# Kernel tuning notes

Hardware: AMD Instinct MI355X
Metric: run time of the kernel (lower is better)

The kernel has to match this reference:

```python
import jax, jax.numpy as jnp
import numpy as np

B, N, X, H = 128, 1023, 256, 256  # N = 2**(D+1)-1 perfect binary trees, root at 0


def _lin_init(key, out_d, in_d, scale=None):
    if scale is None:
        scale = 1.0 / np.sqrt(in_d)
    kw, kb = jax.random.split(key)
    W = jax.random.uniform(kw, (out_d, in_d), jnp.float32, -scale, scale)
    b = jax.random.uniform(kb, (out_d,), jnp.float32, -scale, scale)
    return W, b


def setup_inputs() -> dict:
    key = jax.random.key(0)
    ks = jax.random.split(key, 16)
    embed = jax.random.normal(ks[0], (B, N, X), jnp.float32)
    Wf, bf = _lin_init(ks[1], H, X + H)
    Wi, bi = _lin_init(ks[2], H, X + H)
    Wu, bu = _lin_init(ks[3], H, X + H)
    Wo, bo = _lin_init(ks[4], H, X + H)
    # extra nn.Parameter biases, initialized to zeros as in the module
    b_f = jnp.zeros((H,), jnp.float32)
    b_i = jnp.zeros((H,), jnp.float32)
    b_u = jnp.zeros((H,), jnp.float32)
    b_o = jnp.zeros((H,), jnp.float32)
    W1, bl1 = _lin_init(ks[5], H, H)
    W2, bl2 = _lin_init(ks[6], H, H)
    W3, bl3 = _lin_init(ks[7], H, H)
    W4, bl4 = _lin_init(ks[8], H, H)
    return {"embed": embed, "Wf": Wf, "bf": bf, "b_f": b_f, "Wi": Wi, "bi": bi,
            "b_i": b_i, "Wu": Wu, "bu": bu, "b_u": b_u, "Wo": Wo, "bo": bo,
            "b_o": b_o, "W1": W1, "bl1": bl1, "W2": W2, "bl2": bl2,
            "W3": W3, "bl3": bl3, "W4": W4, "bl4": bl4}


def _tree_lstm(embed, Wf, bf, b_f, Wi, bi, b_i, Wu, bu, b_u, Wo, bo, b_o):
    Bn, Nn, Xn = embed.shape
    Hn = Wf.shape[0]
    D = int(np.log2(Nn + 1)) - 1  # leaf level index
    h = jnp.zeros((Bn, Nn, Hn), embed.dtype)
    c = jnp.zeros((Bn, Nn, Hn), embed.dtype)
    # initial (leaf) level: no children -> h_sum = 0, c_tilde = 0 (apply_node_func on init state)
    i_g = jax.nn.sigmoid(bi + b_i)
    u_g = jnp.tanh(bu + b_u)
    c_leaf = i_g * u_g
    h_leaf = jax.nn.sigmoid(bo + b_o) * jnp.tanh(c_leaf)
    ls, lc = 2 ** D - 1, 2 ** D
    h = h.at[:, ls:ls + lc].set(jnp.broadcast_to(h_leaf, (Bn, lc, Hn)))
    c = c.at[:, ls:ls + lc].set(jnp.broadcast_to(c_leaf, (Bn, lc, Hn)))
    # level-by-level leaf->root; children of node n are 2n+1, 2n+2 (contiguous per level)
    for l in range(D - 1, -1, -1):
        s, cnt = 2 ** l - 1, 2 ** l
        cs, ccnt = 2 ** (l + 1) - 1, 2 ** (l + 1)
        ch_h = h[:, cs:cs + ccnt]        # [B, 2*cnt, H]
        ch_c = c[:, cs:cs + ccnt]
        ch_e = embed[:, cs:cs + ccnt]
        # message: cat([h, embed]); reduce: sum over the 2 children
        msg = jnp.concatenate([ch_h, ch_e], axis=-1).reshape(Bn, cnt, 2, Hn + Xn)
        h_sum = msg.sum(axis=2)                                   # [B, cnt, H+X]
        c_sum = ch_c.reshape(Bn, cnt, 2, Hn).sum(axis=2)          # [B, cnt, H]
        f = jax.nn.sigmoid(h_sum @ Wf.T + bf + b_f)
        c_tilde = f * c_sum  # f broadcast over children: f*(c1+c2) == sum_k f*c_k
        i_gate = jax.nn.sigmoid(h_sum @ Wi.T + bi + b_i)
        u = jnp.tanh(h_sum @ Wu.T + bu + b_u)
        c_new = i_gate * u + c_tilde
        o = jax.nn.sigmoid(h_sum @ Wo.T + bo + b_o)
        h_new = o * jnp.tanh(c_new)
        h = h.at[:, s:s + cnt].set(h_new)
        c = c.at[:, s:s + cnt].set(c_new)
    return h[:, 0]  # root hidden state, [B, H]


def reference(embed, Wf, bf, b_f, Wi, bi, b_i, Wu, bu, b_u, Wo, bo, b_o,
              W1, bl1, W2, bl2, W3, bl3, W4, bl4):
    hr = _tree_lstm(embed, Wf, bf, b_f, Wi, bi, b_i, Wu, bu, b_u, Wo, bo, b_o)
    # dropout is identity in eval mode
    y = jnp.tanh(hr @ W1.T + bl1)
    y2 = jax.nn.relu(hr @ W2.T + bl2) @ W3.T + bl3
    return jax.nn.relu((y + y2) @ W4.T + bl4)
```

## Files before the change

### kernel.cpp

```cpp
#include <hip/hip_runtime.h>

#define HD 256
#define KD 512

typedef _Float16 half8 __attribute__((ext_vector_type(8)));
typedef _Float16 half2v __attribute__((ext_vector_type(2)));
typedef _Float16 half4v __attribute__((ext_vector_type(4)));
typedef float floatx4 __attribute__((ext_vector_type(4)));
typedef float floatx2 __attribute__((ext_vector_type(2)));

__device__ __forceinline__ float sigmf_(float x) { return 1.f / (1.f + __expf(-x)); }
__device__ __forceinline__ float tanhf_(float x) {
  x = fminf(fmaxf(x, -15.f), 15.f);
  float e = __expf(2.f * x);
  return (e - 1.f) / (e + 1.f);
}

__global__ void prep_kernel(const float* __restrict__ bf_, const float* __restrict__ b_f,
                            const float* __restrict__ bi_, const float* __restrict__ b_i,
                            const float* __restrict__ bu_, const float* __restrict__ b_u,
                            const float* __restrict__ bo_, const float* __restrict__ b_o,
                            const float* __restrict__ Wf, const float* __restrict__ Wi,
                            const float* __restrict__ Wu, const float* __restrict__ Wo,
                            float* __restrict__ bsum, float* __restrict__ bias2,
                            float* __restrict__ cleaf2)
{
  __shared__ float hl2[HD];
  __shared__ float part[64][4];
  const int t = threadIdx.x;
  float sf = bf_[t] + b_f[t];
  float si = bi_[t] + b_i[t];
  float su = bu_[t] + b_u[t];
  float so = bo_[t] + b_o[t];
  float ig = 1.f / (1.f + expf(-si));
  float uu = tanhf(su);
  float cl = ig * uu;
  float hl = (1.f / (1.f + expf(-so))) * tanhf(cl);
  hl2[t] = 2.f * hl;
  if (blockIdx.x == 0) {
    bsum[t] = sf; bsum[HD + t] = si; bsum[2 * HD + t] = su; bsum[3 * HD + t] = so;
    cleaf2[t] = cl + cl;
  }
  __syncthreads();
  const int g = blockIdx.x >> 2, q = blockIdx.x & 3;
  const int nl = t >> 2, kq = t & 3;
  const float* Wg = (g == 0) ? Wf : (g == 1) ? Wi : (g == 2) ? Wu : Wo;
  const float* w = Wg + (long)(q * 64 + nl) * KD + kq * 64;
  float s = 0.f;
  for (int k = 0; k < 64; k += 4) {
    floatx4 wv = *(const floatx4*)(w + k);
    floatx4 hv = *(const floatx4*)(&hl2[kq * 64 + k]);
    s += wv[0] * hv[0] + wv[1] * hv[1] + wv[2] * hv[2] + wv[3] * hv[3];
  }
  part[nl][kq] = s;
  __syncthreads();
  if (kq == 0) {
    const int n = q * 64 + nl;
    float tot = part[nl][0] + part[nl][1] + part[nl][2] + part[nl][3];
    float bg = (g == 0) ? (bf_[n] + b_f[n]) : (g == 1) ? (bi_[n] + b_i[n])
             : (g == 2) ? (bu_[n] + b_u[n]) : (bo_[n] + b_o[n]);
    bias2[g * HD + n] = bg + tot;
  }
}

__global__ void wcvt_kernel(const float* __restrict__ Wf, const float* __restrict__ Wi,
                            const float* __restrict__ Wu, const float* __restrict__ Wo,
                            _Float16* __restrict__ Wh)
{
  int idx = (blockIdx.x * 256 + threadIdx.x) * 4;
  int g = idx >> 17;
  int rem = idx & ((1 << 17) - 1);
  const float* src = (g == 0) ? Wf : (g == 1) ? Wi : (g == 2) ? Wu : Wo;
  floatx4 v = *(const floatx4*)(src + rem);
  half4v o;
  o[0] = (_Float16)v[0]; o[1] = (_Float16)v[1]; o[2] = (_Float16)v[2]; o[3] = (_Float16)v[3];
  *(half4v*)(Wh + idx) = o;
}

__global__ void esum_kernel(const float* __restrict__ embed, _Float16* __restrict__ esum)
{
  const int task = blockIdx.x * 256 + threadIdx.x;
  if (task >= 511 * 32) return;
  const int b = blockIdx.y;
  const int p = task >> 5, g8 = task & 31;
  const float* e0 = embed + ((long)b * 1023 + 2 * p + 1) * 256 + g8 * 8;
  const float* e1 = e0 + 256;
  floatx4 x0 = *(const floatx4*)(e0);
  floatx4 x1 = *(const floatx4*)(e0 + 4);
  floatx4 y0 = *(const floatx4*)(e1);
  floatx4 y1 = *(const floatx4*)(e1 + 4);
  half8 s;
#pragma unroll
  for (int e = 0; e < 4; ++e) { s[e] = (_Float16)(x0[e] + y0[e]); s[4 + e] = (_Float16)(x1[e] + y1[e]); }
  *(half8*)(esum + ((long)b * 511 + p) * 256 + g8 * 8) = s;
}

__global__ __launch_bounds__(256, 2)
void level_kernel(const _Float16* __restrict__ hsum_in,
                  const float* __restrict__ csum_in,
                  const _Float16* __restrict__ esum,
                  const _Float16* __restrict__ Wh,
                  const float* __restrict__ bias,
                  _Float16* __restrict__ hsum_out,
                  float* __restrict__ csum_out,
                  int l, int leaf, int fin)
{
  __shared__ _Float16 As[128][256];

  const int cb = blockIdx.y;
  const int m0 = blockIdx.x * 128;
  const int t = threadIdx.x;
  const int wave = t >> 6;
  const int lane = t & 63;
  const int lm = lane & 15;
  const int quad = lane >> 4;
  const int rh = wave >> 1;
  const int ch = wave & 1;
  const int ncol = cb * 32 + ch * 16 + lm;

  floatx4 acc[4][4] = {};

  const int srow0 = t >> 3;
  const int sg = t & 7;

  const _Float16* wb = Wh + (long)ncol * KD + quad * 8;

  auto gemm_chunk = [&](int kbase) {
    half8 bcur[4], bnxt[4];
#pragma unroll
    for (int g = 0; g < 4; ++g)
      bcur[g] = *(const half8*)(wb + (long)g * HD * KD + kbase);
#pragma unroll
    for (int ks = 0; ks < 8; ++ks) {
      if (ks < 7) {
#pragma unroll
        for (int g = 0; g < 4; ++g)
          bnxt[g] = *(const half8*)(wb + (long)g * HD * KD + kbase + (ks + 1) * 32);
      }
      half8 afr[4];
#pragma unroll
      for (int mt = 0; mt < 4; ++mt) {
        int row = rh * 64 + mt * 16 + lm;
        afr[mt] = *(const half8*)(&As[row][(((ks * 4 + quad) ^ (row & 7)) * 8)]);
      }
#pragma unroll
      for (int mt = 0; mt < 4; ++mt)
#pragma unroll
        for (int g = 0; g < 4; ++g)
          acc[mt][g] = __builtin_amdgcn_mfma_f32_16x16x32_f16(afr[mt], bcur[g], acc[mt][g], 0, 0, 0);
#pragma unroll
      for (int g = 0; g < 4; ++g) bcur[g] = bnxt[g];
    }
  };

  const int msk = (1 << l) - 1;

  if (!leaf) {
#pragma unroll
    for (int p = 0; p < 4; ++p) {
      const int r = srow0 + 32 * p;
      const _Float16* src = hsum_in + (long)(m0 + r) * HD;
#pragma unroll
      for (int q = 0; q < 4; ++q) {
        int g8 = sg + 8 * q;
        *(half8*)(&As[r][((g8 ^ (r & 7)) * 8)]) = *(const half8*)(src + g8 * 8);
      }
    }
    __syncthreads();
    gemm_chunk(0);
    __syncthreads();
  }

  {
#pragma unroll
    for (int p = 0; p < 4; ++p) {
      const int r = srow0 + 32 * p;
      const int sm = m0 + r;
      const long erow = (long)(sm >> l) * 511 + msk + (sm & msk);
      const _Float16* src = esum + erow * HD;
#pragma unroll
      for (int q = 0; q < 4; ++q) {
        int g8 = sg + 8 * q;
        *(half8*)(&As[r][((g8 ^ (r & 7)) * 8)]) = *(const half8*)(src + g8 * 8);
      }
    }
  }
  __syncthreads();
  gemm_chunk(256);

  const float b0 = bias[ncol];
  const float b1 = bias[HD + ncol];
  const float b2 = bias[2 * HD + ncol];
  const float b3 = bias[3 * HD + ncol];
  const float clv = leaf ? csum_in[ncol] : 0.f;

#pragma unroll
  for (int mt = 0; mt < 4; ++mt) {
    const int mg0 = m0 + rh * 64 + mt * 16 + quad * 4;
    float hv[4], cvv[4];
#pragma unroll
    for (int e = 0; e < 4; ++e) {
      float cs = leaf ? clv : csum_in[(long)(mg0 + e) * HD + ncol];
      float zf = acc[mt][0][e] + b0;
      float zi = acc[mt][1][e] + b1;
      float zu = acc[mt][2][e] + b2;
      float zo = acc[mt][3][e] + b3;
      float f = sigmf_(zf), ig = sigmf_(zi), uu = tanhf_(zu), oo = sigmf_(zo);
      float cn = ig * uu + f * cs;
      cvv[e] = cn;
      hv[e] = oo * tanhf_(cn);
    }
    if (fin) {
#pragma unroll
      for (int e = 0; e < 4; ++e)
        hsum_out[(long)(mg0 + e) * HD + ncol] = (_Float16)hv[e];
    } else {
      const long pr = mg0 >> 1;
      hsum_out[pr * HD + ncol] = (_Float16)(hv[0] + hv[1]);
      hsum_out[(pr + 1) * HD + ncol] = (_Float16)(hv[2] + hv[3]);
      csum_out[pr * HD + ncol] = cvv[0] + cvv[1];
      csum_out[(pr + 1) * HD + ncol] = cvv[2] + cvv[3];
    }
  }
}

__global__ void head_all_kernel(const _Float16* __restrict__ hr,
                                const float* __restrict__ W1, const float* __restrict__ bl1,
                                const float* __restrict__ W2, const float* __restrict__ bl2,
                                const float* __restrict__ W3, const float* __restrict__ bl3,
                                const float* __restrict__ W4, const float* __restrict__ bl4,
                                float* __restrict__ out)
{
  __shared__ float a[HD];
  __shared__ float t1s[HD];
  __shared__ float t2s[HD];
  int b = blockIdx.x, n = threadIdx.x;
  a[n] = (float)hr[b * HD + n];
  __syncthreads();
  {
    const float* w1 = W1 + n * HD;
    const float* w2 = W2 + n * HD;
    float s1 = bl1[n], s2 = bl2[n];
    for (int k = 0; k < HD; k += 4) {
      floatx4 av = *(const floatx4*)(&a[k]);
      floatx4 w1v = *(const floatx4*)(w1 + k);
      floatx4 w2v = *(const floatx4*)(w2 + k);
#pragma unroll
      for (int e = 0; e < 4; ++e) { s1 += av[e] * w1v[e]; s2 += av[e] * w2v[e]; }
    }
    t1s[n] = tanhf_(s1);
    t2s[n] = fmaxf(s2, 0.f);
  }
  __syncthreads();
  {
    const float* w3 = W3 + n * HD;
    float s3 = bl3[n];
    for (int k = 0; k < HD; k += 4) {
      floatx4 av = *(const floatx4*)(&t2s[k]);
      floatx4 wv = *(const floatx4*)(w3 + k);
#pragma unroll
      for (int e = 0; e < 4; ++e) s3 += av[e] * wv[e];
    }
    __syncthreads();
    a[n] = t1s[n] + s3;
  }
  __syncthreads();
  {
    const float* w4 = W4 + n * HD;
    float s4 = bl4[n];
    for (int k = 0; k < HD; k += 4) {
      floatx4 av = *(const floatx4*)(&a[k]);
      floatx4 wv = *(const floatx4*)(w4 + k);
#pragma unroll
      for (int e = 0; e < 4; ++e) s4 += av[e] * wv[e];
    }
    out[b * HD + n] = fmaxf(s4, 0.f);
  }
}

extern "C" void kernel_launch(void* const* d_in, const int* in_sizes, int n_in,
                              void* d_out, int out_size, void* d_ws, size_t ws_size,
                              hipStream_t stream)
{
  (void)in_sizes; (void)n_in; (void)out_size; (void)ws_size;
  const float* embed = (const float*)d_in[0];
  const float* Wf  = (const float*)d_in[1];
  const float* bf_ = (const float*)d_in[2];
  const float* b_f = (const float*)d_in[3];
  const float* Wi  = (const float*)d_in[4];
  const float* bi_ = (const float*)d_in[5];
  const float* b_i = (const float*)d_in[6];
  const float* Wu  = (const float*)d_in[7];
  const float* bu_ = (const float*)d_in[8];
  const float* b_u = (const float*)d_in[9];
  const float* Wo  = (const float*)d_in[10];
  const float* bo_ = (const float*)d_in[11];
  const float* b_o = (const float*)d_in[12];
  const float* W1  = (const float*)d_in[13];
  const float* bl1 = (const float*)d_in[14];
  const float* W2  = (const float*)d_in[15];
  const float* bl2 = (const float*)d_in[16];
  const float* W3  = (const float*)d_in[17];
  const float* bl3 = (const float*)d_in[18];
  const float* W4  = (const float*)d_in[19];
  const float* bl4 = (const float*)d_in[20];

  char* ws = (char*)d_ws;
  _Float16* Wh   = (_Float16*)(ws);
  float* bsum    = (float*)(ws + 1048576);
  float* bias2   = (float*)(ws + 1052672);
  float* cleaf2  = (float*)(ws + 1056768);
  _Float16* hr   = (_Float16*)(ws + 1057792);
  _Float16* esum = (_Float16*)(ws + 1123328);
  _Float16* HsA  = (_Float16*)(ws + 34612224);
  float* CsA     = (float*)(ws + 43000832);
  _Float16* HsB  = (_Float16*)(ws + 59778048);
  float* CsB     = (float*)(ws + 63972352);

  prep_kernel<<<dim3(16), dim3(256), 0, stream>>>(bf_, b_f, bi_, b_i, bu_, b_u, bo_, b_o,
                                                  Wf, Wi, Wu, Wo, bsum, bias2, cleaf2);
  wcvt_kernel<<<dim3(512), dim3(256), 0, stream>>>(Wf, Wi, Wu, Wo, Wh);
  esum_kernel<<<dim3(64, 128), dim3(256), 0, stream>>>(embed, esum);

  _Float16* hbufs[2] = {HsA, HsB};
  float* cbufs[2] = {CsA, CsB};
  int pp = 0;
  const _Float16* hin = nullptr;
  const float* cin = cleaf2;
  for (int l = 8; l >= 0; --l) {
    const int leaf = (l == 8);
    const int fin = (l == 0);
    _Float16* hout = fin ? hr : hbufs[pp];
    float* cout = cbufs[pp];
    dim3 grid(1 << l, 8);
    level_kernel<<<grid, dim3(256), 0, stream>>>(hin, cin, esum, Wh,
                                                 leaf ? bias2 : bsum,
                                                 hout, cout, l, leaf, fin);
    hin = hbufs[pp];
    cin = cbufs[pp];
    pp ^= 1;
  }

  head_all_kernel<<<dim3(128), dim3(256), 0, stream>>>(hr, W1, bl1, W2, bl2, W3, bl3,
                                                       W4, bl4, (float*)d_out);
}
```

Measured before the change: 485.5 us.

## Widen level tiles to 128x64 and fuse top six tree levels per batch

```diff
diff --git a/kernel.cpp b/kernel.cpp
--- a/kernel.cpp
+++ b/kernel.cpp
@@ -4,10 +4,8 @@
 #define KD 512
 
 typedef _Float16 half8 __attribute__((ext_vector_type(8)));
-typedef _Float16 half2v __attribute__((ext_vector_type(2)));
 typedef _Float16 half4v __attribute__((ext_vector_type(4)));
 typedef float floatx4 __attribute__((ext_vector_type(4)));
-typedef float floatx2 __attribute__((ext_vector_type(2)));
 
 __device__ __forceinline__ float sigmf_(float x) { return 1.f / (1.f + __expf(-x)); }
 __device__ __forceinline__ float tanhf_(float x) {
@@ -96,14 +94,14 @@
 }
 
 __global__ __launch_bounds__(256, 2)
-void level_kernel(const _Float16* __restrict__ hsum_in,
-                  const float* __restrict__ csum_in,
-                  const _Float16* __restrict__ esum,
-                  const _Float16* __restrict__ Wh,
-                  const float* __restrict__ bias,
-                  _Float16* __restrict__ hsum_out,
-                  float* __restrict__ csum_out,
-                  int l, int leaf, int fin)
+void level_kernel_w(const _Float16* __restrict__ hsum_in,
+                    const float* __restrict__ csum_in,
+                    const _Float16* __restrict__ esum,
+                    const _Float16* __restrict__ Wh,
+                    const float* __restrict__ bias,
+                    _Float16* __restrict__ hsum_out,
+                    float* __restrict__ csum_out,
+                    int l, int leaf)
 {
   __shared__ _Float16 As[128][256];
 
@@ -114,11 +112,9 @@
   const int lane = t & 63;
   const int lm = lane & 15;
   const int quad = lane >> 4;
-  const int rh = wave >> 1;
-  const int ch = wave & 1;
-  const int ncol = cb * 32 + ch * 16 + lm;
-
-  floatx4 acc[4][4] = {};
+  const int ncol = cb * 64 + wave * 16 + lm;
+
+  floatx4 acc[8][4] = {};
 
   const int srow0 = t >> 3;
   const int sg = t & 7;
@@ -137,14 +133,14 @@
         for (int g = 0; g < 4; ++g)
           bnxt[g] = *(const half8*)(wb + (long)g * HD * KD + kbase + (ks + 1) * 32);
       }
-      half8 afr[4];
-#pragma unroll
-      for (int mt = 0; mt < 4; ++mt) {
-        int row = rh * 64 + mt * 16 + lm;
+      half8 afr[8];
+#pragma unroll
+      for (int mt = 0; mt < 8; ++mt) {
+        int row = mt * 16 + lm;
         afr[mt] = *(const half8*)(&As[row][(((ks * 4 + quad) ^ (row & 7)) * 8)]);
       }
 #pragma unroll
-      for (int mt = 0; mt < 4; ++mt)
+      for (int mt = 0; mt < 8; ++mt)
 #pragma unroll
         for (int g = 0; g < 4; ++g)
           acc[mt][g] = __builtin_amdgcn_mfma_f32_16x16x32_f16(afr[mt], bcur[g], acc[mt][g], 0, 0, 0);
@@ -171,18 +167,16 @@
     __syncthreads();
   }
 
-  {
-#pragma unroll
-    for (int p = 0; p < 4; ++p) {
-      const int r = srow0 + 32 * p;
-      const int sm = m0 + r;
-      const long erow = (long)(sm >> l) * 511 + msk + (sm & msk);
-      const _Float16* src = esum + erow * HD;
-#pragma unroll
-      for (int q = 0; q < 4; ++q) {
-        int g8 = sg + 8 * q;
-        *(half8*)(&As[r][((g8 ^ (r & 7)) * 8)]) = *(const half8*)(src + g8 * 8);
-      }
+#pragma unroll
+  for (int p = 0; p < 4; ++p) {
+    const int r = srow0 + 32 * p;
+    const int sm = m0 + r;
+    const long erow = (long)(sm >> l) * 511 + msk + (sm & msk);
+    const _Float16* src = esum + erow * HD;
+#pragma unroll
+    for (int q = 0; q < 4; ++q) {
+      int g8 = sg + 8 * q;
+      *(half8*)(&As[r][((g8 ^ (r & 7)) * 8)]) = *(const half8*)(src + g8 * 8);
     }
   }
   __syncthreads();
@@ -195,8 +189,8 @@
   const float clv = leaf ? csum_in[ncol] : 0.f;
 
 #pragma unroll
-  for (int mt = 0; mt < 4; ++mt) {
-    const int mg0 = m0 + rh * 64 + mt * 16 + quad * 4;
+  for (int mt = 0; mt < 8; ++mt) {
+    const int mg0 = m0 + mt * 16 + quad * 4;
     float hv[4], cvv[4];
 #pragma unroll
     for (int e = 0; e < 4; ++e) {
@@ -210,17 +204,142 @@
       cvv[e] = cn;
       hv[e] = oo * tanhf_(cn);
     }
-    if (fin) {
-#pragma unroll
-      for (int e = 0; e < 4; ++e)
-        hsum_out[(long)(mg0 + e) * HD + ncol] = (_Float16)hv[e];
-    } else {
-      const long pr = mg0 >> 1;
-      hsum_out[pr * HD + ncol] = (_Float16)(hv[0] + hv[1]);
-      hsum_out[(pr + 1) * HD + ncol] = (_Float16)(hv[2] + hv[3]);
-      csum_out[pr * HD + ncol] = cvv[0] + cvv[1];
-      csum_out[(pr + 1) * HD + ncol] = cvv[2] + cvv[3];
-    }
+    const long pr = mg0 >> 1;
+    hsum_out[pr * HD + ncol] = (_Float16)(hv[0] + hv[1]);
+    hsum_out[(pr + 1) * HD + ncol] = (_Float16)(hv[2] + hv[3]);
+    csum_out[pr * HD + ncol] = cvv[0] + cvv[1];
+    csum_out[(pr + 1) * HD + ncol] = cvv[2] + cvv[3];
+  }
+}
+
+__global__ __launch_bounds__(256, 1)
+void tail_kernel(const _Float16* __restrict__ Hs_in,
+                 const _Float16* __restrict__ esum,
+                 const _Float16* __restrict__ Wh,
+                 const float* __restrict__ bsum,
+                 float* __restrict__ CsA, float* __restrict__ CsB,
+                 _Float16* __restrict__ hr)
+{
+  __shared__ _Float16 eL[63][256];
+  __shared__ _Float16 hL[2][32][256];
+
+  const int b = blockIdx.x;
+  const int t = threadIdx.x;
+  const int wave = t >> 6;
+  const int lane = t & 63;
+  const int lm = lane & 15;
+  const int quad = lane >> 4;
+
+  for (int idx = t; idx < 63 * 32; idx += 256) {
+    const int p = idx >> 5, kg = idx & 31;
+    *(half8*)(&eL[p][((kg ^ (p & 7)) * 8)]) =
+        *(const half8*)(esum + ((long)b * 511 + p) * 256 + kg * 8);
+  }
+  for (int idx = t; idx < 32 * 32; idx += 256) {
+    const int r = idx >> 5, kg = idx & 31;
+    *(half8*)(&hL[0][r][((kg ^ (r & 7)) * 8)]) =
+        *(const half8*)(Hs_in + ((long)b * 32 + r) * 256 + kg * 8);
+  }
+  __syncthreads();
+
+  float* cb[2] = {CsA, CsB};
+  int ci = 0;
+  int hp = 0;
+
+  for (int l = 5; l >= 0; --l) {
+    const int R = 1 << l;
+    const int msk = R - 1;
+    const int fin = (l == 0);
+    const int two = (l == 5);
+    const float* cin = cb[ci];
+    float* cout = cb[ci ^ 1];
+
+    for (int ct = 0; ct < 4; ++ct) {
+      const int ncol = wave * 64 + ct * 16 + lm;
+      const _Float16* wb = Wh + (long)ncol * KD + quad * 8;
+      floatx4 acc0[4] = {};
+      floatx4 acc1[4] = {};
+      half8 bcur[4], bnxt[4];
+#pragma unroll
+      for (int g = 0; g < 4; ++g)
+        bcur[g] = *(const half8*)(wb + (long)g * HD * KD);
+#pragma unroll
+      for (int ks = 0; ks < 16; ++ks) {
+        if (ks < 15) {
+#pragma unroll
+          for (int g = 0; g < 4; ++g)
+            bnxt[g] = *(const half8*)(wb + (long)g * HD * KD + (ks + 1) * 32);
+        }
+        half8 a0, a1;
+        if (ks < 8) {
+          const int kg = ks * 4 + quad;
+          a0 = *(const half8*)(&hL[hp][lm][((kg ^ (lm & 7)) * 8)]);
+          if (two) {
+            const int r1 = 16 + lm;
+            a1 = *(const half8*)(&hL[hp][r1][((kg ^ (r1 & 7)) * 8)]);
+          }
+        } else {
+          const int kg = (ks - 8) * 4 + quad;
+          const int p0 = msk + lm;
+          a0 = *(const half8*)(&eL[p0][((kg ^ (p0 & 7)) * 8)]);
+          if (two) {
+            const int p1 = msk + 16 + lm;
+            a1 = *(const half8*)(&eL[p1][((kg ^ (p1 & 7)) * 8)]);
+          }
+        }
+#pragma unroll
+        for (int g = 0; g < 4; ++g)
+          acc0[g] = __builtin_amdgcn_mfma_f32_16x16x32_f16(a0, bcur[g], acc0[g], 0, 0, 0);
+        if (two) {
+#pragma unroll
+          for (int g = 0; g < 4; ++g)
+            acc1[g] = __builtin_amdgcn_mfma_f32_16x16x32_f16(a1, bcur[g], acc1[g], 0, 0, 0);
+        }
+#pragma unroll
+        for (int g = 0; g < 4; ++g) bcur[g] = bnxt[g];
+      }
+
+      const float b0 = bsum[ncol];
+      const float b1 = bsum[HD + ncol];
+      const float b2 = bsum[2 * HD + ncol];
+      const float b3 = bsum[3 * HD + ncol];
+
+      auto epi = [&](const floatx4 (&ac)[4], int mg0) {
+        float hv[4], cvv[4];
+#pragma unroll
+        for (int e = 0; e < 4; ++e) {
+          float cs = cin[((long)b * R + mg0 + e) * HD + ncol];
+          float zf = ac[0][e] + b0;
+          float zi = ac[1][e] + b1;
+          float zu = ac[2][e] + b2;
+          float zo = ac[3][e] + b3;
+          float f = sigmf_(zf), ig = sigmf_(zi), uu = tanhf_(zu), oo = sigmf_(zo);
+          float cn = ig * uu + f * cs;
+          cvv[e] = cn;
+          hv[e] = oo * tanhf_(cn);
+        }
+        if (fin) {
+          if (mg0 == 0) hr[b * HD + ncol] = (_Float16)hv[0];
+        } else {
+          const int pr = mg0 >> 1;
+          if (mg0 < R) {
+            hL[hp ^ 1][pr][(((ncol >> 3) ^ (pr & 7)) * 8) + (ncol & 7)] =
+                (_Float16)(hv[0] + hv[1]);
+            cout[((long)b * (R >> 1) + pr) * HD + ncol] = cvv[0] + cvv[1];
+          }
+          if (mg0 + 2 < R) {
+            hL[hp ^ 1][pr + 1][(((ncol >> 3) ^ ((pr + 1) & 7)) * 8) + (ncol & 7)] =
+                (_Float16)(hv[2] + hv[3]);
+            cout[((long)b * (R >> 1) + pr + 1) * HD + ncol] = cvv[2] + cvv[3];
+          }
+        }
+      };
+      epi(acc0, quad * 4);
+      if (two) epi(acc1, 16 + quad * 4);
+    }
+    __syncthreads();
+    hp ^= 1;
+    ci ^= 1;
   }
 }
 
@@ -322,24 +441,14 @@
   wcvt_kernel<<<dim3(512), dim3(256), 0, stream>>>(Wf, Wi, Wu, Wo, Wh);
   esum_kernel<<<dim3(64, 128), dim3(256), 0, stream>>>(embed, esum);
 
-  _Float16* hbufs[2] = {HsA, HsB};
-  float* cbufs[2] = {CsA, CsB};
-  int pp = 0;
-  const _Float16* hin = nullptr;
-  const float* cin = cleaf2;
-  for (int l = 8; l >= 0; --l) {
-    const int leaf = (l == 8);
-    const int fin = (l == 0);
-    _Float16* hout = fin ? hr : hbufs[pp];
-    float* cout = cbufs[pp];
-    dim3 grid(1 << l, 8);
-    level_kernel<<<grid, dim3(256), 0, stream>>>(hin, cin, esum, Wh,
-                                                 leaf ? bias2 : bsum,
-                                                 hout, cout, l, leaf, fin);
-    hin = hbufs[pp];
-    cin = cbufs[pp];
-    pp ^= 1;
-  }
+  level_kernel_w<<<dim3(256, 4), dim3(256), 0, stream>>>(nullptr, cleaf2, esum, Wh,
+                                                         bias2, HsA, CsA, 8, 1);
+  level_kernel_w<<<dim3(128, 4), dim3(256), 0, stream>>>(HsA, CsA, esum, Wh,
+                                                         bsum, HsB, CsB, 7, 0);
+  level_kernel_w<<<dim3(64, 4), dim3(256), 0, stream>>>(HsB, CsB, esum, Wh,
+                                                        bsum, HsA, CsA, 6, 0);
+  tail_kernel<<<dim3(128), dim3(256), 0, stream>>>(HsA, esum, Wh, bsum,
+                                                   CsA, CsB, hr);
 
   head_all_kernel<<<dim3(128), dim3(256), 0, stream>>>(hr, W1, bl1, W2, bl2, W3, bl3,
                                                        W4, bl4, (float*)d_out);
```

Result: slower. 568.6 us (+17.1%).
